# Kernel tuning notes

Hardware: AMD Instinct MI355X
Metric: run time of the kernel (lower is better)

The kernel has to match this reference:

```python
import jax, jax.numpy as jnp
import numpy as np

NUM_QUBITS = 13
NUM_LAYERS = 2


def setup_inputs() -> dict:
    key = jax.random.key(0)
    k1, k2 = jax.random.split(key)
    x = jax.random.normal(k1, (512, 2 ** NUM_QUBITS), dtype=jnp.float32)
    weights = jax.random.normal(k2, (NUM_LAYERS, NUM_QUBITS, 3), dtype=jnp.float32)
    return {"x": x, "weights": weights}


def _rot_matrix(phi, theta, omega):
    # qml.Rot(phi, theta, omega) = RZ(omega) @ RY(theta) @ RZ(phi)
    c = jnp.cos(theta * 0.5).astype(jnp.complex64)
    s = jnp.sin(theta * 0.5).astype(jnp.complex64)
    e_m = jnp.exp((-0.5j) * (phi + omega).astype(jnp.complex64))
    e_p = jnp.exp((0.5j) * (phi + omega).astype(jnp.complex64))
    e_d = jnp.exp((0.5j) * (phi - omega).astype(jnp.complex64))
    e_dc = jnp.exp((-0.5j) * (phi - omega).astype(jnp.complex64))
    row0 = jnp.stack([e_m * c, -e_d * s])
    row1 = jnp.stack([e_dc * s, e_p * c])
    return jnp.stack([row0, row1])  # (2, 2) complex64


def _apply_1q(psi, U, q):
    # psi: (B, 2, 2, ..., 2); contract qubit axis q with 2x2 gate U
    ax = 1 + q
    psi = jnp.moveaxis(psi, ax, -1)
    psi = psi @ U.T
    return jnp.moveaxis(psi, -1, ax)


def _apply_cnot(psi, c, t):
    # X on target where control bit == 1
    s0 = jax.lax.index_in_dim(psi, 0, axis=1 + c, keepdims=True)
    s1 = jax.lax.index_in_dim(psi, 1, axis=1 + c, keepdims=True)
    s1 = jnp.flip(s1, axis=1 + t)
    return jnp.concatenate([s0, s1], axis=1 + c)


def reference(x, weights):
    n = NUM_QUBITS
    B = x.shape[0]
    # AmplitudeEmbedding with normalize=True
    norm = jnp.sqrt(jnp.sum(x * x, axis=1, keepdims=True))
    psi = (x / norm).astype(jnp.complex64).reshape((B,) + (2,) * n)
    # StronglyEntanglingLayers (default ranges r_l = (l % (n-1)) + 1, CNOT imprimitive)
    for l in range(NUM_LAYERS):
        r = (l % (n - 1)) + 1
        for q in range(n):
            U = _rot_matrix(weights[l, q, 0], weights[l, q, 1], weights[l, q, 2])
            psi = _apply_1q(psi, U, q)
        for q in range(n):
            psi = _apply_cnot(psi, q, (q + r) % n)
    # expval(PauliZ(n // 2)) = p(bit=0) - p(bit=1)
    m = n // 2
    probs = jnp.real(psi) ** 2 + jnp.imag(psi) ** 2
    axes = tuple(i for i in range(1, n + 1) if i != 1 + m)
    p = probs.sum(axis=axes)  # (B, 2)
    return p[:, 0] - p[:, 1]
```

## Files before the change

### kernel.cpp

```cpp
#include <hip/hip_runtime.h>
#include <math.h>

#define NQ    13
#define DIM   8192
#define BLOCK 512
#define NGATE 26


__device__ __forceinline__ int SW(int a) { return a ^ (((a >> 7) & 7) << 2); }

struct PCols { int c[NQ]; };
constexpr PCols make_cols(int r) {
    PCols P{};
    for (int b = 0; b < NQ; ++b) {
        int cc = 1 << b;
        for (int cq = 0; cq < NQ; ++cq) {
            const int cb = 12 - cq;
            const int tb = 12 - ((cq + r) % NQ);
            cc ^= ((cc >> cb) & 1) << tb;
        }
        P.c[b] = cc;
    }
    return P;
}
constexpr PCols C1 = make_cols(1);
constexpr int make_rm6() {
    int m = 0;
    for (int b = 0; b < NQ; ++b) m |= ((make_cols(2).c[b] >> 6) & 1) << b;
    return m;
}
constexpr int RM6 = make_rm6();

struct Combos { int k[16]; };
constexpr Combos make_combos() {
    Combos K{};
    for (int j = 0; j < 16; ++j)
        K.k[j] = ((j & 1) ? C1.c[0] : 0) ^ ((j & 2) ? C1.c[1] : 0)
               ^ ((j & 4) ? C1.c[10] : 0) ^ ((j & 8) ? C1.c[11] : 0);
    return K;
}
constexpr Combos KC = make_combos();

constexpr int make_sjw() {
    int wv = 0;
    for (int j = 0; j < 16; ++j) {
        const int jm = (j & 3) | (((j >> 2) & 3) << 10);
        wv |= (__builtin_popcount(jm & RM6) & 1) << j;
    }
    return wv;
}
constexpr int SJW = make_sjw();

__device__ __forceinline__ float2 f2mul(float s, float2 a) {
    return make_float2(s * a.x, s * a.y);
}
__device__ __forceinline__ float2 f2fma(float s, float2 a, float2 b) {
    return make_float2(fmaf(s, a.x, b.x), fmaf(s, a.y, b.y));
}
__device__ __forceinline__ float2 fswap(float2 a) { return make_float2(-a.y, a.x); }

struct G8 { float4 a, b; };
__device__ __forceinline__ G8 ldg8(const float* gm, int gi) {
    G8 g;
    g.a = *(const float4*)&gm[gi * 8];
    g.b = *(const float4*)&gm[gi * 8 + 4];
    return g;
}

template<int P>
__device__ __forceinline__ void rotp(float2* c, const G8 g) {
    #pragma unroll
    for (int m = 0; m < 8; ++m) {
        const int j0 = ((m >> P) << (P + 1)) | (m & ((1 << P) - 1));
        const int j1 = j0 | (1 << P);
        const float2 a0 = c[j0], a1 = c[j1];
        const float2 s0 = fswap(a0), s1 = fswap(a1);
        c[j0] = f2fma(g.a.w, s1, f2fma(g.a.z, a1, f2fma(g.a.y, s0, f2mul(g.a.x, a0))));
        c[j1] = f2fma(g.b.w, s1, f2fma(g.b.z, a1, f2fma(g.b.y, s0, f2mul(g.b.x, a0))));
    }
}

template<int CTRL>
__device__ __forceinline__ float dppx(float v) {
    return __int_as_float(
        __builtin_amdgcn_update_dpp(0, __float_as_int(v), CTRL, 0xf, 0xf, true));
}
template<int CTRL>
__device__ __forceinline__ void rotlane(float2* c, const G8 g, const bool hi) {
    const float Ar = hi ? g.b.z : g.a.x;
    const float Ai = hi ? g.b.w : g.a.y;
    const float Br = hi ? g.b.x : g.a.z;
    const float Bi = hi ? g.b.y : g.a.w;
    #pragma unroll
    for (int j = 0; j < 16; ++j) {
        const float2 p  = make_float2(dppx<CTRL>(c[j].x), dppx<CTRL>(c[j].y));
        const float2 so = fswap(c[j]), sp = fswap(p);
        c[j] = f2fma(Bi, sp, f2fma(Br, p, f2fma(Ai, so, f2mul(Ar, c[j]))));
    }
}

__device__ __forceinline__ void loadgrp(const float* re, const float* im, int a, float2* c) {
    const float4 r = *(const float4*)&re[a];
    const float4 i = *(const float4*)&im[a];
    c[0] = make_float2(r.x, i.x); c[1] = make_float2(r.y, i.y);
    c[2] = make_float2(r.z, i.z); c[3] = make_float2(r.w, i.w);
}
__device__ __forceinline__ void storegrp(float* re, float* im, int a, const float2* c) {
    *(float4*)&re[a] = make_float4(c[0].x, c[1].x, c[2].x, c[3].x);
    *(float4*)&im[a] = make_float4(c[0].y, c[1].y, c[2].y, c[3].y);
}

__global__ __launch_bounds__(BLOCK, 4) void qsim_kernel(
    const float* __restrict__ x,
    const float* __restrict__ w,
    float* __restrict__ out)
{
    __shared__ __align__(16) float re[DIM];
    __shared__ __align__(16) float im[DIM];
    __shared__ __align__(16) float gm[NGATE * 8];
    __shared__ float red_ss[8], red_acc[8];

    const int b = blockIdx.x;
    const int t = threadIdx.x;

    if (t < NGATE) {
        const float phi = w[t * 3 + 0], theta = w[t * 3 + 1], omega = w[t * 3 + 2];
        float co, si;  sincosf(0.5f * theta, &si, &co);
        float sps, cps, sds, cds;
        sincosf(0.5f * (phi + omega), &sps, &cps);
        sincosf(0.5f * (phi - omega), &sds, &cds);
        float* g = &gm[t * 8];
        g[0] =  cps * co;  g[1] = -sps * co;
        g[2] = -cds * si;  g[3] = -sds * si;
        g[4] =  cds * si;  g[5] = -sds * si;
        g[6] =  cps * co;  g[7] =  sps * co;
    }

    const float4* x4 = (const float4*)(x + (size_t)b * DIM);
    float ss = 0.f;
    #pragma unroll
    for (int k = 0; k < 4; ++k) {
        const int m = t + BLOCK * k;
        const int a = SW(4 * m);
        const float4 v = x4[m];
        *(float4*)&re[a] = v;
        ss += v.x * v.x + v.y * v.y + v.z * v.z + v.w * v.w;
    }
    #pragma unroll
    for (int off = 32; off > 0; off >>= 1) ss += __shfl_down(ss, off, 64);
    if ((t & 63) == 0) red_ss[t >> 6] = ss;
    __syncthreads();
    float total = 0.f;
    #pragma unroll
    for (int i = 0; i < 8; ++i) total += red_ss[i];

    float2 c[16];

    const int base2 = (((t >> 2) & 15) << 2) | ((t & 3) << 8) | (((t >> 6) & 7) << 10);
    const int base3 = (((t >> 1) & 255) << 2) | ((t & 1) << 12);

    #pragma unroll
    for (int l = 0; l < 2; ++l) {
        const int G = l * 13;

        if (l == 0) {
            #pragma unroll
            for (int g = 0; g < 4; ++g) {
                const float4 r = *(const float4*)&re[SW((t << 4) | (g << 2))];
                c[4 * g + 0] = make_float2(r.x, 0.f);
                c[4 * g + 1] = make_float2(r.y, 0.f);
                c[4 * g + 2] = make_float2(r.z, 0.f);
                c[4 * g + 3] = make_float2(r.w, 0.f);
            }
        } else {
            #pragma unroll
            for (int g = 0; g < 4; ++g)
                loadgrp(re, im, SW((t << 4) | (g << 2)), &c[4 * g]);
        }
        rotp<0>(c, ldg8(gm, G + 12));
        rotp<1>(c, ldg8(gm, G + 11));
        rotp<2>(c, ldg8(gm, G + 10));
        rotp<3>(c, ldg8(gm, G +  9));
        rotlane<0xB1>(c, ldg8(gm, G + 8), (t & 1) != 0);
        rotlane<0x4E>(c, ldg8(gm, G + 7), (t & 2) != 0);
        #pragma unroll
        for (int g = 0; g < 4; ++g)
            storegrp(re, im, SW((t << 4) | (g << 2)), &c[4 * g]);
        __syncthreads();

        #pragma unroll
        for (int h = 0; h < 4; ++h) loadgrp(re, im, SW(base2 | (h << 6)), &c[4 * h]);
        rotp<2>(c, ldg8(gm, G + 6));
        rotp<3>(c, ldg8(gm, G + 5));
        rotlane<0xB1>(c, ldg8(gm, G + 4), (t & 1) != 0);
        rotlane<0x4E>(c, ldg8(gm, G + 3), (t & 2) != 0);
        #pragma unroll
        for (int h = 0; h < 4; ++h) storegrp(re, im, SW(base2 | (h << 6)), &c[4 * h]);
        __syncthreads();

        #pragma unroll
        for (int h = 0; h < 4; ++h) loadgrp(re, im, SW(base3 | (h << 10)), &c[4 * h]);
        if (l == 0) __syncthreads();
        rotp<2>(c, ldg8(gm, G + 2));
        rotp<3>(c, ldg8(gm, G + 1));
        rotlane<0xB1>(c, ldg8(gm, G + 0), (t & 1) != 0);

        if (l == 0) {
            int mb = 0;
            if (t & 1) mb ^= C1.c[12];
            #pragma unroll
            for (int bb = 0; bb < 8; ++bb)
                if ((t >> (bb + 1)) & 1) mb ^= C1.c[2 + bb];
            #pragma unroll
            for (int j = 0; j < 16; ++j) {
                const int a = SW(mb ^ KC.k[j]);
                re[a] = c[j].x; im[a] = c[j].y;
            }
            __syncthreads();
        }
    }

    const int sbase = __popc(base3 & RM6) & 1;
    float acc = 0.f;
    #pragma unroll
    for (int j = 0; j < 16; ++j) {
        const float p = c[j].x * c[j].x + c[j].y * c[j].y;
        acc += (sbase ^ ((SJW >> j) & 1)) ? -p : p;
    }
    #pragma unroll
    for (int off = 32; off > 0; off >>= 1) acc += __shfl_down(acc, off, 64);
    if ((t & 63) == 0) red_acc[t >> 6] = acc;
    __syncthreads();
    if (t == 0) {
        float tot = 0.f;
        #pragma unroll
        for (int i = 0; i < 8; ++i) tot += red_acc[i];
        out[b] = tot / total;
    }
}

extern "C" void kernel_launch(void* const* d_in, const int* in_sizes, int n_in,
                              void* d_out, int out_size, void* d_ws, size_t ws_size,
                              hipStream_t stream) {
    const float* x = (const float*)d_in[0];
    const float* w = (const float*)d_in[1];
    float* out = (float*)d_out;
    const int B = in_sizes[0] / DIM;
    qsim_kernel<<<B, BLOCK, 0, stream>>>(x, w, out);
}
```

Before: 84.38 us.

## Precompute gate matrices in a prep kernel and use packed float2 vector math

```diff
diff --git a/kernel.cpp b/kernel.cpp
--- a/kernel.cpp
+++ b/kernel.cpp
@@ -6,6 +6,8 @@
 #define BLOCK 512
 #define NGATE 26
 
+
+typedef float v2f __attribute__((ext_vector_type(2)));
 
 __device__ __forceinline__ int SW(int a) { return a ^ (((a >> 7) & 7) << 2); }
 
@@ -51,90 +53,81 @@
 }
 constexpr int SJW = make_sjw();
 
-__device__ __forceinline__ float2 f2mul(float s, float2 a) {
-    return make_float2(s * a.x, s * a.y);
-}
-__device__ __forceinline__ float2 f2fma(float s, float2 a, float2 b) {
-    return make_float2(fmaf(s, a.x, b.x), fmaf(s, a.y, b.y));
-}
-__device__ __forceinline__ float2 fswap(float2 a) { return make_float2(-a.y, a.x); }
-
 struct G8 { float4 a, b; };
-__device__ __forceinline__ G8 ldg8(const float* gm, int gi) {
-    G8 g;
-    g.a = *(const float4*)&gm[gi * 8];
-    g.b = *(const float4*)&gm[gi * 8 + 4];
-    return g;
-}
-
-template<int P>
-__device__ __forceinline__ void rotp(float2* c, const G8 g) {
-    #pragma unroll
-    for (int m = 0; m < 8; ++m) {
-        const int j0 = ((m >> P) << (P + 1)) | (m & ((1 << P) - 1));
-        const int j1 = j0 | (1 << P);
-        const float2 a0 = c[j0], a1 = c[j1];
-        const float2 s0 = fswap(a0), s1 = fswap(a1);
-        c[j0] = f2fma(g.a.w, s1, f2fma(g.a.z, a1, f2fma(g.a.y, s0, f2mul(g.a.x, a0))));
-        c[j1] = f2fma(g.b.w, s1, f2fma(g.b.z, a1, f2fma(g.b.y, s0, f2mul(g.b.x, a0))));
-    }
-}
-
-template<int CTRL>
-__device__ __forceinline__ float dppx(float v) {
-    return __int_as_float(
-        __builtin_amdgcn_update_dpp(0, __float_as_int(v), CTRL, 0xf, 0xf, true));
-}
-template<int CTRL>
-__device__ __forceinline__ void rotlane(float2* c, const G8 g, const bool hi) {
-    const float Ar = hi ? g.b.z : g.a.x;
-    const float Ai = hi ? g.b.w : g.a.y;
-    const float Br = hi ? g.b.x : g.a.z;
-    const float Bi = hi ? g.b.y : g.a.w;
-    #pragma unroll
-    for (int j = 0; j < 16; ++j) {
-        const float2 p  = make_float2(dppx<CTRL>(c[j].x), dppx<CTRL>(c[j].y));
-        const float2 so = fswap(c[j]), sp = fswap(p);
-        c[j] = f2fma(Bi, sp, f2fma(Br, p, f2fma(Ai, so, f2mul(Ar, c[j]))));
-    }
-}
-
-__device__ __forceinline__ void loadgrp(const float* re, const float* im, int a, float2* c) {
-    const float4 r = *(const float4*)&re[a];
-    const float4 i = *(const float4*)&im[a];
-    c[0] = make_float2(r.x, i.x); c[1] = make_float2(r.y, i.y);
-    c[2] = make_float2(r.z, i.z); c[3] = make_float2(r.w, i.w);
-}
-__device__ __forceinline__ void storegrp(float* re, float* im, int a, const float2* c) {
-    *(float4*)&re[a] = make_float4(c[0].x, c[1].x, c[2].x, c[3].x);
-    *(float4*)&im[a] = make_float4(c[0].y, c[1].y, c[2].y, c[3].y);
-}
-
-__global__ __launch_bounds__(BLOCK, 4) void qsim_kernel(
-    const float* __restrict__ x,
-    const float* __restrict__ w,
-    float* __restrict__ out)
-{
-    __shared__ __align__(16) float re[DIM];
-    __shared__ __align__(16) float im[DIM];
-    __shared__ __align__(16) float gm[NGATE * 8];
-    __shared__ float red_ss[8], red_acc[8];
-
-    const int b = blockIdx.x;
+
+__global__ void prep_gates(const float* __restrict__ w, G8* __restrict__ gw) {
     const int t = threadIdx.x;
-
     if (t < NGATE) {
         const float phi = w[t * 3 + 0], theta = w[t * 3 + 1], omega = w[t * 3 + 2];
         float co, si;  sincosf(0.5f * theta, &si, &co);
         float sps, cps, sds, cds;
         sincosf(0.5f * (phi + omega), &sps, &cps);
         sincosf(0.5f * (phi - omega), &sds, &cds);
-        float* g = &gm[t * 8];
-        g[0] =  cps * co;  g[1] = -sps * co;
-        g[2] = -cds * si;  g[3] = -sds * si;
-        g[4] =  cds * si;  g[5] = -sds * si;
-        g[6] =  cps * co;  g[7] =  sps * co;
-    }
+        G8 g;
+        g.a = make_float4(cps * co, -sps * co, -cds * si, -sds * si);
+        g.b = make_float4(cds * si, -sds * si,  cps * co,  sps * co);
+        gw[t] = g;
+    }
+}
+
+__device__ __forceinline__ v2f cswap(v2f a) { return (v2f){ -a.y, a.x }; }
+
+template<int P>
+__device__ __forceinline__ void rotp(v2f* c, const G8 g) {
+    #pragma unroll
+    for (int m = 0; m < 8; ++m) {
+        const int j0 = ((m >> P) << (P + 1)) | (m & ((1 << P) - 1));
+        const int j1 = j0 | (1 << P);
+        const v2f a0 = c[j0], a1 = c[j1];
+        const v2f s0 = cswap(a0), s1 = cswap(a1);
+        c[j0] = g.a.x * a0 + g.a.y * s0 + g.a.z * a1 + g.a.w * s1;
+        c[j1] = g.b.x * a0 + g.b.y * s0 + g.b.z * a1 + g.b.w * s1;
+    }
+}
+
+template<int CTRL>
+__device__ __forceinline__ float dppx(float v) {
+    return __int_as_float(
+        __builtin_amdgcn_update_dpp(0, __float_as_int(v), CTRL, 0xf, 0xf, true));
+}
+template<int CTRL>
+__device__ __forceinline__ void rotlane(v2f* c, const G8 g, const bool hi) {
+    const float Ar = hi ? g.b.z : g.a.x;
+    const float Ai = hi ? g.b.w : g.a.y;
+    const float Br = hi ? g.b.x : g.a.z;
+    const float Bi = hi ? g.b.y : g.a.w;
+    #pragma unroll
+    for (int j = 0; j < 16; ++j) {
+        v2f p;
+        p.x = dppx<CTRL>(c[j].x);
+        p.y = dppx<CTRL>(c[j].y);
+        const v2f so = cswap(c[j]), sp = cswap(p);
+        c[j] = Ar * c[j] + Ai * so + Br * p + Bi * sp;
+    }
+}
+
+__device__ __forceinline__ void loadgrp(const float* re, const float* im, int a, v2f* c) {
+    const float4 r = *(const float4*)&re[a];
+    const float4 i = *(const float4*)&im[a];
+    c[0] = (v2f){ r.x, i.x }; c[1] = (v2f){ r.y, i.y };
+    c[2] = (v2f){ r.z, i.z }; c[3] = (v2f){ r.w, i.w };
+}
+__device__ __forceinline__ void storegrp(float* re, float* im, int a, const v2f* c) {
+    *(float4*)&re[a] = make_float4(c[0].x, c[1].x, c[2].x, c[3].x);
+    *(float4*)&im[a] = make_float4(c[0].y, c[1].y, c[2].y, c[3].y);
+}
+
+__global__ __launch_bounds__(BLOCK, 4) void qsim_kernel(
+    const float* __restrict__ x,
+    const G8* __restrict__ gw,
+    float* __restrict__ out)
+{
+    __shared__ __align__(16) float re[DIM];
+    __shared__ __align__(16) float im[DIM];
+    __shared__ float red_ss[8], red_acc[8];
+
+    const int b = blockIdx.x;
+    const int t = threadIdx.x;
 
     const float4* x4 = (const float4*)(x + (size_t)b * DIM);
     float ss = 0.f;
@@ -154,7 +147,7 @@
     #pragma unroll
     for (int i = 0; i < 8; ++i) total += red_ss[i];
 
-    float2 c[16];
+    v2f c[16];
 
     const int base2 = (((t >> 2) & 15) << 2) | ((t & 3) << 8) | (((t >> 6) & 7) << 10);
     const int base3 = (((t >> 1) & 255) << 2) | ((t & 1) << 12);
@@ -167,22 +160,22 @@
             #pragma unroll
             for (int g = 0; g < 4; ++g) {
                 const float4 r = *(const float4*)&re[SW((t << 4) | (g << 2))];
-                c[4 * g + 0] = make_float2(r.x, 0.f);
-                c[4 * g + 1] = make_float2(r.y, 0.f);
-                c[4 * g + 2] = make_float2(r.z, 0.f);
-                c[4 * g + 3] = make_float2(r.w, 0.f);
+                c[4 * g + 0] = (v2f){ r.x, 0.f };
+                c[4 * g + 1] = (v2f){ r.y, 0.f };
+                c[4 * g + 2] = (v2f){ r.z, 0.f };
+                c[4 * g + 3] = (v2f){ r.w, 0.f };
             }
         } else {
             #pragma unroll
             for (int g = 0; g < 4; ++g)
                 loadgrp(re, im, SW((t << 4) | (g << 2)), &c[4 * g]);
         }
-        rotp<0>(c, ldg8(gm, G + 12));
-        rotp<1>(c, ldg8(gm, G + 11));
-        rotp<2>(c, ldg8(gm, G + 10));
-        rotp<3>(c, ldg8(gm, G +  9));
-        rotlane<0xB1>(c, ldg8(gm, G + 8), (t & 1) != 0);
-        rotlane<0x4E>(c, ldg8(gm, G + 7), (t & 2) != 0);
+        rotp<0>(c, gw[G + 12]);
+        rotp<1>(c, gw[G + 11]);
+        rotp<2>(c, gw[G + 10]);
+        rotp<3>(c, gw[G +  9]);
+        rotlane<0xB1>(c, gw[G + 8], (t & 1) != 0);
+        rotlane<0x4E>(c, gw[G + 7], (t & 2) != 0);
         #pragma unroll
         for (int g = 0; g < 4; ++g)
             storegrp(re, im, SW((t << 4) | (g << 2)), &c[4 * g]);
@@ -190,10 +183,10 @@
 
         #pragma unroll
         for (int h = 0; h < 4; ++h) loadgrp(re, im, SW(base2 | (h << 6)), &c[4 * h]);
-        rotp<2>(c, ldg8(gm, G + 6));
-        rotp<3>(c, ldg8(gm, G + 5));
-        rotlane<0xB1>(c, ldg8(gm, G + 4), (t & 1) != 0);
-        rotlane<0x4E>(c, ldg8(gm, G + 3), (t & 2) != 0);
+        rotp<2>(c, gw[G + 6]);
+        rotp<3>(c, gw[G + 5]);
+        rotlane<0xB1>(c, gw[G + 4], (t & 1) != 0);
+        rotlane<0x4E>(c, gw[G + 3], (t & 2) != 0);
         #pragma unroll
         for (int h = 0; h < 4; ++h) storegrp(re, im, SW(base2 | (h << 6)), &c[4 * h]);
         __syncthreads();
@@ -201,9 +194,9 @@
         #pragma unroll
         for (int h = 0; h < 4; ++h) loadgrp(re, im, SW(base3 | (h << 10)), &c[4 * h]);
         if (l == 0) __syncthreads();
-        rotp<2>(c, ldg8(gm, G + 2));
-        rotp<3>(c, ldg8(gm, G + 1));
-        rotlane<0xB1>(c, ldg8(gm, G + 0), (t & 1) != 0);
+        rotp<2>(c, gw[G + 2]);
+        rotp<3>(c, gw[G + 1]);
+        rotlane<0xB1>(c, gw[G + 0], (t & 1) != 0);
 
         if (l == 0) {
             int mb = 0;
@@ -245,6 +238,8 @@
     const float* x = (const float*)d_in[0];
     const float* w = (const float*)d_in[1];
     float* out = (float*)d_out;
+    G8* gw = (G8*)d_ws;
     const int B = in_sizes[0] / DIM;
-    qsim_kernel<<<B, BLOCK, 0, stream>>>(x, w, out);
-}
+    prep_gates<<<1, 64, 0, stream>>>(w, gw);
+    qsim_kernel<<<B, BLOCK, 0, stream>>>(x, (const G8*)gw, out);
+}
```

Measured after the change: 93.82 us. 11.2% more time.
